# Optimization experiments

Measured on AMD Instinct MI355X. Metric: run time of the kernel, lower is better.

The kernel has to match this reference:

```python
import jax, jax.numpy as jnp
import numpy as np

B, IN, H = 4096, 1024, 1024


def setup_inputs() -> dict:
    key = jax.random.key(0)
    ks = jax.random.split(key, 12)
    s = float(np.sqrt(6.0 / (IN + H)))  # xavier-uniform-like scale
    u = lambda k, shp: jax.random.uniform(k, shp, jnp.float32, -s, s)
    return {
        "x": jax.random.normal(ks[0], (B, IN), jnp.float32),
        "h_prev": jax.random.normal(ks[1], (B, H), jnp.float32),
        "c_prev": jax.random.normal(ks[2], (B, H), jnp.float32),
        "n_prev": jnp.ones((B, H), jnp.float32),
        "m_prev": jnp.zeros((B, H), jnp.float32),
        "Wi_x": u(ks[3], (H, IN)), "bi": jnp.zeros((H,), jnp.float32), "Wi_h": u(ks[4], (H, H)),
        "Wf_x": u(ks[5], (H, IN)), "bf": jnp.full((H,), 2.0, jnp.float32), "Wf_h": u(ks[6], (H, H)),
        "Wz_x": u(ks[7], (H, IN)), "bz": jnp.zeros((H,), jnp.float32), "Wz_h": u(ks[8], (H, H)),
        "Wo_x": u(ks[9], (H, IN)), "bo": jnp.zeros((H,), jnp.float32), "Wo_h": u(ks[10], (H, H)),
    }


def reference(x, h_prev, c_prev, n_prev, m_prev,
              Wi_x, bi, Wi_h, Wf_x, bf, Wf_h,
              Wz_x, bz, Wz_h, Wo_x, bo, Wo_h):
    # 8 projections (x-side with bias, h-side without), torch Linear: y = x @ W.T + b
    i_tilde = x @ Wi_x.T + bi + h_prev @ Wi_h.T
    f_aff   = x @ Wf_x.T + bf + h_prev @ Wf_h.T
    z_aff   = x @ Wz_x.T + bz + h_prev @ Wz_h.T
    o_aff   = x @ Wo_x.T + bo + h_prev @ Wo_h.T

    # forget_as_exp=False path: sigmoid forget gate, log-domain stabilizer
    log_f = jnp.log(jnp.clip(jax.nn.sigmoid(f_aff), 1e-8, None))
    m_t = jnp.maximum(log_f + m_prev, i_tilde)
    i_prime = jnp.exp(i_tilde - m_t)
    f_prime = jnp.exp(log_f + m_prev - m_t)

    z = jnp.tanh(z_aff)
    c_t = f_prime * c_prev + i_prime * z
    n_t = f_prime * n_prev + i_prime
    h_t = jax.nn.sigmoid(o_aff) * (c_t / jnp.clip(n_t, 1e-6, None))
    return h_t, c_t, n_t, m_t
```

## Files before the change

kernel.cpp:

```cpp
#include <hip/hip_runtime.h>
#include <stdint.h>


#define B_DIM 4096
#define K_DIM 2048
#define TM 128
#define TN 128
#define BK 32

typedef __bf16 bf16x8 __attribute__((ext_vector_type(8)));
typedef float f32x4 __attribute__((ext_vector_type(4)));
typedef unsigned short ushort8 __attribute__((ext_vector_type(8)));

__device__ __forceinline__ unsigned short f2bf(float f) {
  unsigned u = __float_as_uint(f);
  u += 0x7fffu + ((u >> 16) & 1u);
  return (unsigned short)(u >> 16);
}
__device__ __forceinline__ float bf2f(unsigned short u) {
  return __uint_as_float(((unsigned)u) << 16);
}

__device__ __forceinline__ void load_lds16(const void* g, void* lds) {
  __builtin_amdgcn_global_load_lds(
      (const __attribute__((address_space(1))) unsigned int*)(uintptr_t)g,
      (__attribute__((address_space(3))) unsigned int*)(unsigned int)(uintptr_t)lds,
      16, 0, 0);
}

__global__ void detect_k(const unsigned* __restrict__ W, const unsigned* __restrict__ xw,
                         const unsigned* __restrict__ npw, const unsigned* __restrict__ bfw,
                         int* __restrict__ flags) {
  int lane = threadIdx.x;
  int vw = 0, vx = 0;
  if (lane < 32) {
    unsigned w = W[lane];
    vw = (((w >> 7) & 0xFFu) > 122u) ? 1 : 0;
  } else {
    unsigned w = xw[lane - 32];
    vx = (((w >> 7) & 0xFFu) > 129u) ? 1 : 0;
  }
  unsigned long long bw = __ballot(vw);
  unsigned long long bx = __ballot(vx);
  if (lane == 0) {
    flags[0] = (bw == 0ull) ? 1 : 0;
    flags[1] = (bx == 0ull) ? 1 : 0;
    flags[2] = (npw[0] == 0x3F803F80u) ? 1 : 0;
    flags[3] = (bfw[0] == 0x40004000u) ? 1 : 0;
  }
}

__device__ __forceinline__ ushort8 load8_as_bf16(const void* base, size_t off, bool isbf) {
  if (isbf) return *(const ushort8*)((const unsigned short*)base + off);
  const float* f = (const float*)base + off;
  float4 v0 = ((const float4*)f)[0];
  float4 v1 = ((const float4*)f)[1];
  ushort8 o;
  o[0] = f2bf(v0.x); o[1] = f2bf(v0.y); o[2] = f2bf(v0.z); o[3] = f2bf(v0.w);
  o[4] = f2bf(v1.x); o[5] = f2bf(v1.y); o[6] = f2bf(v1.z); o[7] = f2bf(v1.w);
  return o;
}

__global__ void pack_A(const void* __restrict__ xv, const void* __restrict__ hv,
                       unsigned short* __restrict__ Apk, const int* __restrict__ flags) {
  bool isbf = flags[1] != 0;
  int t = blockIdx.x * blockDim.x + threadIdx.x;
  int base = t * 8;
  int m = base >> 11;
  int k = base & 2047;
  size_t off = (size_t)m * 1024 + (k & 1023);
  const void* src = (k < 1024) ? xv : hv;
  *(ushort8*)(Apk + base) = load8_as_bf16(src, off, isbf);
}

__global__ void pack_B(const void* __restrict__ Wix, const void* __restrict__ Wih,
                       const void* __restrict__ Wfx, const void* __restrict__ Wfh,
                       const void* __restrict__ Wzx, const void* __restrict__ Wzh,
                       const void* __restrict__ Wox, const void* __restrict__ Woh,
                       unsigned short* __restrict__ Bpk, const int* __restrict__ flags) {
  bool isbf = flags[0] != 0;
  int t = blockIdx.x * blockDim.x + threadIdx.x;
  int base = t * 8;
  int p = base >> 11;
  int k = base & 2047;
  int g = (p >> 4) & 3;
  int n = ((p >> 6) << 4) | (p & 15);
  const void* W;
  if (k < 1024) W = (g == 0) ? Wix : (g == 1) ? Wfx : (g == 2) ? Wzx : Wox;
  else          W = (g == 0) ? Wih : (g == 1) ? Wfh : (g == 2) ? Wzh : Woh;
  size_t off = (size_t)n * 1024 + (k & 1023);
  *(ushort8*)(Bpk + base) = load8_as_bf16(W, off, isbf);
}

__global__ __launch_bounds__(256) void gemm_fused(
    const unsigned short* __restrict__ Apk,
    const unsigned short* __restrict__ Bpk,
    const void* __restrict__ bi, const void* __restrict__ bfg,
    const void* __restrict__ bz, const void* __restrict__ bo,
    const void* __restrict__ c_prev, const void* __restrict__ n_prev,
    const void* __restrict__ m_prev,
    float* __restrict__ out,
    const int* __restrict__ flags)
{
  __shared__ unsigned short As[TM * BK];
  __shared__ unsigned short Bs[TN * BK];

  const int tid  = threadIdx.x;
  const int wave = tid >> 6;
  const int lane = tid & 63;
  const int wr = wave >> 1;
  const int wc = wave & 1;
  const int qrow = lane >> 4;
  const int col  = lane & 15;

  const int m0 = blockIdx.x * TM;
  const int p0 = blockIdx.y * TN;

  f32x4 acc[4][4] = {};

  for (int k0 = 0; k0 < K_DIM; k0 += BK) {
    __syncthreads();
#pragma unroll
    for (int q = 0; q < 2; ++q) {
      int c = wave * 128 + q * 64 + lane;
      int row = c >> 2;
      int cb = c & 3;
      const unsigned short* gA = Apk + (size_t)(m0 + row) * K_DIM + k0 + cb * 8;
      const unsigned short* gB = Bpk + (size_t)(p0 + row) * K_DIM + k0 + cb * 8;
      load_lds16(gA, (void*)(As + (size_t)(wave * 128 + q * 64) * 8));
      load_lds16(gB, (void*)(Bs + (size_t)(wave * 128 + q * 64) * 8));
    }
    __syncthreads();

    bf16x8 af[4], bfr[4];
#pragma unroll
    for (int t = 0; t < 4; ++t) {
      af[t]  = *(const bf16x8*)(As + (wr * 64 + t * 16 + col) * BK + qrow * 8);
      bfr[t] = *(const bf16x8*)(Bs + (wc * 64 + t * 16 + col) * BK + qrow * 8);
    }
#pragma unroll
    for (int ti = 0; ti < 4; ++ti)
#pragma unroll
      for (int tj = 0; tj < 4; ++tj)
        acc[ti][tj] = __builtin_amdgcn_mfma_f32_16x16x32_bf16(af[ti], bfr[tj], acc[ti][tj], 0, 0, 0);
  }

  const bool sbf = flags[2] != 0;
  const bool bbf = flags[3] != 0;
  const int n = (blockIdx.y * 2 + wc) * 16 + col;
  const float bi_n = bbf ? bf2f(((const unsigned short*)bi)[n])  : ((const float*)bi)[n];
  const float bf_n = bbf ? bf2f(((const unsigned short*)bfg)[n]) : ((const float*)bfg)[n];
  const float bz_n = bbf ? bf2f(((const unsigned short*)bz)[n])  : ((const float*)bz)[n];
  const float bo_n = bbf ? bf2f(((const unsigned short*)bo)[n])  : ((const float*)bo)[n];
  const int rowbase = m0 + wr * 64 + qrow * 4;

  float* out_h = out;
  float* out_c = out + 4194304;
  float* out_n = out + 2 * 4194304;
  float* out_m = out + 3 * 4194304;

#pragma unroll
  for (int ti = 0; ti < 4; ++ti) {
#pragma unroll
    for (int r = 0; r < 4; ++r) {
      int row = rowbase + ti * 16 + r;
      int idx = row * 1024 + n;
      float it = acc[ti][0][r] + bi_n;
      float fa = acc[ti][1][r] + bf_n;
      float za = acc[ti][2][r] + bz_n;
      float oa = acc[ti][3][r] + bo_n;
      float cp  = sbf ? bf2f(((const unsigned short*)c_prev)[idx]) : ((const float*)c_prev)[idx];
      float npv = sbf ? bf2f(((const unsigned short*)n_prev)[idx]) : ((const float*)n_prev)[idx];
      float mp  = sbf ? bf2f(((const unsigned short*)m_prev)[idx]) : ((const float*)m_prev)[idx];

      float sf = 1.f / (1.f + __expf(-fa));
      sf = fmaxf(sf, 1e-8f);
      float lf = __logf(sf);
      float mt = fmaxf(lf + mp, it);
      float ip = __expf(it - mt);
      float fp = __expf(lf + mp - mt);
      float zc = fminf(fmaxf(za, -15.f), 15.f);
      float e2 = __expf(2.f * zc);
      float z  = (e2 - 1.f) / (e2 + 1.f);
      float ct = fp * cp + ip * z;
      float nt = fp * npv + ip;
      float so = 1.f / (1.f + __expf(-oa));
      float ht = so * (ct / fmaxf(nt, 1e-6f));

      out_h[idx] = ht;
      out_c[idx] = ct;
      out_n[idx] = nt;
      out_m[idx] = mt;
    }
  }
}

extern "C" void kernel_launch(void* const* d_in, const int* in_sizes, int n_in,
                              void* d_out, int out_size, void* d_ws, size_t ws_size,
                              hipStream_t stream) {
  const void* x      = d_in[0];
  const void* h_prev = d_in[1];
  const void* c_prev = d_in[2];
  const void* n_prev = d_in[3];
  const void* m_prev = d_in[4];
  const void* Wi_x = d_in[5];
  const void* bi   = d_in[6];
  const void* Wi_h = d_in[7];
  const void* Wf_x = d_in[8];
  const void* bf   = d_in[9];
  const void* Wf_h = d_in[10];
  const void* Wz_x = d_in[11];
  const void* bz   = d_in[12];
  const void* Wz_h = d_in[13];
  const void* Wo_x = d_in[14];
  const void* bo   = d_in[15];
  const void* Wo_h = d_in[16];

  int* flags = (int*)d_ws;
  unsigned short* Apk = (unsigned short*)((char*)d_ws + 256);
  unsigned short* Bpk = Apk + (size_t)B_DIM * K_DIM;

  detect_k<<<1, 64, 0, stream>>>((const unsigned*)Wi_x, (const unsigned*)x,
                                 (const unsigned*)n_prev, (const unsigned*)bf, flags);

  int nthreads = B_DIM * K_DIM / 8;
  pack_A<<<nthreads / 256, 256, 0, stream>>>(x, h_prev, Apk, flags);
  pack_B<<<nthreads / 256, 256, 0, stream>>>(Wi_x, Wi_h, Wf_x, Wf_h,
                                             Wz_x, Wz_h, Wo_x, Wo_h, Bpk, flags);
  dim3 grid(B_DIM / TM, 4096 / TN);
  gemm_fused<<<grid, 256, 0, stream>>>(Apk, Bpk, bi, bf, bz, bo,
                                       c_prev, n_prev, m_prev,
                                       (float*)d_out, flags);
}
```

Before: 296.4 us.

## Double-buffer GEMM LDS tiles with swizzle and merge detect/pack kernels into one

New measurement: 293.6 us. About the same (-0.9%).

```diff
diff --git a/kernel.cpp b/kernel.cpp
--- a/kernel.cpp
+++ b/kernel.cpp
@@ -26,28 +26,6 @@
       (const __attribute__((address_space(1))) unsigned int*)(uintptr_t)g,
       (__attribute__((address_space(3))) unsigned int*)(unsigned int)(uintptr_t)lds,
       16, 0, 0);
-}
-
-__global__ void detect_k(const unsigned* __restrict__ W, const unsigned* __restrict__ xw,
-                         const unsigned* __restrict__ npw, const unsigned* __restrict__ bfw,
-                         int* __restrict__ flags) {
-  int lane = threadIdx.x;
-  int vw = 0, vx = 0;
-  if (lane < 32) {
-    unsigned w = W[lane];
-    vw = (((w >> 7) & 0xFFu) > 122u) ? 1 : 0;
-  } else {
-    unsigned w = xw[lane - 32];
-    vx = (((w >> 7) & 0xFFu) > 129u) ? 1 : 0;
-  }
-  unsigned long long bw = __ballot(vw);
-  unsigned long long bx = __ballot(vx);
-  if (lane == 0) {
-    flags[0] = (bw == 0ull) ? 1 : 0;
-    flags[1] = (bx == 0ull) ? 1 : 0;
-    flags[2] = (npw[0] == 0x3F803F80u) ? 1 : 0;
-    flags[3] = (bfw[0] == 0x40004000u) ? 1 : 0;
-  }
 }
 
 __device__ __forceinline__ ushort8 load8_as_bf16(const void* base, size_t off, bool isbf) {
@@ -61,35 +39,44 @@
   return o;
 }
 
-__global__ void pack_A(const void* __restrict__ xv, const void* __restrict__ hv,
-                       unsigned short* __restrict__ Apk, const int* __restrict__ flags) {
-  bool isbf = flags[1] != 0;
-  int t = blockIdx.x * blockDim.x + threadIdx.x;
-  int base = t * 8;
-  int m = base >> 11;
-  int k = base & 2047;
-  size_t off = (size_t)m * 1024 + (k & 1023);
-  const void* src = (k < 1024) ? xv : hv;
-  *(ushort8*)(Apk + base) = load8_as_bf16(src, off, isbf);
-}
-
-__global__ void pack_B(const void* __restrict__ Wix, const void* __restrict__ Wih,
-                       const void* __restrict__ Wfx, const void* __restrict__ Wfh,
-                       const void* __restrict__ Wzx, const void* __restrict__ Wzh,
-                       const void* __restrict__ Wox, const void* __restrict__ Woh,
-                       unsigned short* __restrict__ Bpk, const int* __restrict__ flags) {
-  bool isbf = flags[0] != 0;
-  int t = blockIdx.x * blockDim.x + threadIdx.x;
-  int base = t * 8;
-  int p = base >> 11;
-  int k = base & 2047;
-  int g = (p >> 4) & 3;
-  int n = ((p >> 6) << 4) | (p & 15);
-  const void* W;
-  if (k < 1024) W = (g == 0) ? Wix : (g == 1) ? Wfx : (g == 2) ? Wzx : Wox;
-  else          W = (g == 0) ? Wih : (g == 1) ? Wfh : (g == 2) ? Wzh : Woh;
-  size_t off = (size_t)n * 1024 + (k & 1023);
-  *(ushort8*)(Bpk + base) = load8_as_bf16(W, off, isbf);
+__global__ void pack_all(const void* __restrict__ xv, const void* __restrict__ hv,
+                         const void* __restrict__ Wix, const void* __restrict__ Wih,
+                         const void* __restrict__ Wfx, const void* __restrict__ Wfh,
+                         const void* __restrict__ Wzx, const void* __restrict__ Wzh,
+                         const void* __restrict__ Wox, const void* __restrict__ Woh,
+                         unsigned short* __restrict__ Apk, unsigned short* __restrict__ Bpk) {
+  const int blk = blockIdx.x;
+  const int lane = threadIdx.x & 63;
+  const bool isA = blk < 4096;
+  const unsigned* disc = (const unsigned*)(isA ? xv : Wix);
+  int v = 0;
+  if (lane < 32) {
+    unsigned e = (disc[lane] >> 7) & 0xFFu;
+    v = (e > (isA ? 129u : 122u)) ? 1 : 0;
+  }
+  const bool isbf = (__ballot(v) == 0ull);
+
+  if (isA) {
+    int t = blk * 256 + threadIdx.x;
+    int base = t * 8;
+    int m = base >> 11;
+    int k = base & 2047;
+    size_t off = (size_t)m * 1024 + (k & 1023);
+    const void* src = (k < 1024) ? xv : hv;
+    *(ushort8*)(Apk + base) = load8_as_bf16(src, off, isbf);
+  } else {
+    int t = (blk - 4096) * 256 + threadIdx.x;
+    int base = t * 8;
+    int p = base >> 11;
+    int k = base & 2047;
+    int g = (p >> 4) & 3;
+    int n = ((p >> 6) << 4) | (p & 15);
+    const void* W;
+    if (k < 1024) W = (g == 0) ? Wix : (g == 1) ? Wfx : (g == 2) ? Wzx : Wox;
+    else          W = (g == 0) ? Wih : (g == 1) ? Wfh : (g == 2) ? Wzh : Woh;
+    size_t off = (size_t)n * 1024 + (k & 1023);
+    *(ushort8*)(Bpk + base) = load8_as_bf16(W, off, isbf);
+  }
 }
 
 __global__ __launch_bounds__(256) void gemm_fused(
@@ -99,11 +86,10 @@
     const void* __restrict__ bz, const void* __restrict__ bo,
     const void* __restrict__ c_prev, const void* __restrict__ n_prev,
     const void* __restrict__ m_prev,
-    float* __restrict__ out,
-    const int* __restrict__ flags)
+    float* __restrict__ out)
 {
-  __shared__ unsigned short As[TM * BK];
-  __shared__ unsigned short Bs[TN * BK];
+  __shared__ unsigned short As[2][TM * BK];
+  __shared__ unsigned short Bs[2][TN * BK];
 
   const int tid  = threadIdx.x;
   const int wave = tid >> 6;
@@ -118,35 +104,46 @@
 
   f32x4 acc[4][4] = {};
 
-  for (int k0 = 0; k0 < K_DIM; k0 += BK) {
-    __syncthreads();
-#pragma unroll
-    for (int q = 0; q < 2; ++q) {
-      int c = wave * 128 + q * 64 + lane;
-      int row = c >> 2;
-      int cb = c & 3;
-      const unsigned short* gA = Apk + (size_t)(m0 + row) * K_DIM + k0 + cb * 8;
-      const unsigned short* gB = Bpk + (size_t)(p0 + row) * K_DIM + k0 + cb * 8;
-      load_lds16(gA, (void*)(As + (size_t)(wave * 128 + q * 64) * 8));
-      load_lds16(gB, (void*)(Bs + (size_t)(wave * 128 + q * 64) * 8));
-    }
-    __syncthreads();
+  const int swz = ((qrow + (col >> 1)) & 3) * 8;
+
+#define STAGE(k0, buf)                                                        \
+  {                                                                           \
+    _Pragma("unroll")                                                         \
+    for (int q = 0; q < 2; ++q) {                                             \
+      int c = wave * 128 + q * 64 + lane;                                     \
+      int row = c >> 2;                                                       \
+      int cb = ((c & 3) - (row >> 1)) & 3;                                    \
+      const unsigned short* gA = Apk + (size_t)(m0 + row) * K_DIM + (k0) + cb * 8; \
+      const unsigned short* gB = Bpk + (size_t)(p0 + row) * K_DIM + (k0) + cb * 8; \
+      load_lds16(gA, (void*)(As[buf] + (wave * 128 + q * 64) * 8));           \
+      load_lds16(gB, (void*)(Bs[buf] + (wave * 128 + q * 64) * 8));           \
+    }                                                                         \
+  }
+
+  STAGE(0, 0);
+  __syncthreads();
+
+  int cur = 0;
+  for (int k0 = 0; k0 < K_DIM; k0 += BK, cur ^= 1) {
+    if (k0 + BK < K_DIM) STAGE(k0 + BK, cur ^ 1);
 
     bf16x8 af[4], bfr[4];
 #pragma unroll
     for (int t = 0; t < 4; ++t) {
-      af[t]  = *(const bf16x8*)(As + (wr * 64 + t * 16 + col) * BK + qrow * 8);
-      bfr[t] = *(const bf16x8*)(Bs + (wc * 64 + t * 16 + col) * BK + qrow * 8);
+      af[t]  = *(const bf16x8*)(As[cur] + (wr * 64 + t * 16 + col) * BK + swz);
+      bfr[t] = *(const bf16x8*)(Bs[cur] + (wc * 64 + t * 16 + col) * BK + swz);
     }
 #pragma unroll
     for (int ti = 0; ti < 4; ++ti)
 #pragma unroll
       for (int tj = 0; tj < 4; ++tj)
         acc[ti][tj] = __builtin_amdgcn_mfma_f32_16x16x32_bf16(af[ti], bfr[tj], acc[ti][tj], 0, 0, 0);
-  }
-
-  const bool sbf = flags[2] != 0;
-  const bool bbf = flags[3] != 0;
+
+    __syncthreads();
+  }
+
+  const bool sbf = (((const unsigned*)n_prev)[0] == 0x3F803F80u);
+  const bool bbf = (((const unsigned*)bfg)[0]    == 0x40004000u);
   const int n = (blockIdx.y * 2 + wc) * 16 + col;
   const float bi_n = bbf ? bf2f(((const unsigned short*)bi)[n])  : ((const float*)bi)[n];
   const float bf_n = bbf ? bf2f(((const unsigned short*)bfg)[n]) : ((const float*)bfg)[n];
@@ -216,19 +213,13 @@
   const void* bo   = d_in[15];
   const void* Wo_h = d_in[16];
 
-  int* flags = (int*)d_ws;
-  unsigned short* Apk = (unsigned short*)((char*)d_ws + 256);
+  unsigned short* Apk = (unsigned short*)d_ws;
   unsigned short* Bpk = Apk + (size_t)B_DIM * K_DIM;
 
-  detect_k<<<1, 64, 0, stream>>>((const unsigned*)Wi_x, (const unsigned*)x,
-                                 (const unsigned*)n_prev, (const unsigned*)bf, flags);
-
-  int nthreads = B_DIM * K_DIM / 8;
-  pack_A<<<nthreads / 256, 256, 0, stream>>>(x, h_prev, Apk, flags);
-  pack_B<<<nthreads / 256, 256, 0, stream>>>(Wi_x, Wi_h, Wf_x, Wf_h,
-                                             Wz_x, Wz_h, Wo_x, Wo_h, Bpk, flags);
+  pack_all<<<8192, 256, 0, stream>>>(x, h_prev, Wi_x, Wi_h, Wf_x, Wf_h,
+                                     Wz_x, Wz_h, Wo_x, Wo_h, Apk, Bpk);
   dim3 grid(B_DIM / TM, 4096 / TN);
   gemm_fused<<<grid, 256, 0, stream>>>(Apk, Bpk, bi, bf, bz, bo,
                                        c_prev, n_prev, m_prev,
-                                       (float*)d_out, flags);
-}
+                                       (float*)d_out);
+}
```
